# Performance work log

Measured on AMD Instinct MI355X. Metric: run time of the kernel, lower is better.

## Reference

```python
import jax, jax.numpy as jnp
import numpy as np

N = 50000      # nodes
E = 800000     # edges (before self-loops)
IN = 512       # in_dim
HID = 128      # hidden_dim
HEADS = 4
NEG_SLOPE = 0.2


def setup_inputs() -> dict:
    key = jax.random.key(0)
    ks = jax.random.split(key, 20)
    s = 0.05
    inp = {
        'x': jax.random.normal(ks[0], (N, IN), jnp.float32),
        'edge_index': jax.random.randint(ks[1], (2, E), 0, N, dtype=jnp.int32),
        # layer 0: GATConv(IN -> HID, heads=HEADS)
        'W0': jax.random.normal(ks[2], (HEADS * HID, IN), jnp.float32) * s,
        'a_src0': jax.random.normal(ks[3], (HEADS, HID), jnp.float32) * s,
        'a_dst0': jax.random.normal(ks[4], (HEADS, HID), jnp.float32) * s,
        'b0': jnp.zeros((HEADS * HID,), jnp.float32),
        # layer 1: GATConv(HEADS*HID -> HID, heads=HEADS)
        'W1': jax.random.normal(ks[5], (HEADS * HID, HEADS * HID), jnp.float32) * s,
        'a_src1': jax.random.normal(ks[6], (HEADS, HID), jnp.float32) * s,
        'a_dst1': jax.random.normal(ks[7], (HEADS, HID), jnp.float32) * s,
        'b1': jnp.zeros((HEADS * HID,), jnp.float32),
        # layer 2: GATConv(HEADS*HID -> HID, heads=1)
        'W2': jax.random.normal(ks[8], (HID, HEADS * HID), jnp.float32) * s,
        'a_src2': jax.random.normal(ks[9], (1, HID), jnp.float32) * s,
        'a_dst2': jax.random.normal(ks[10], (1, HID), jnp.float32) * s,
        'b2': jnp.zeros((HID,), jnp.float32),
        # output heads
        'Wv': jax.random.normal(ks[11], (HID, HID), jnp.float32) * s,
        'bv': jnp.zeros((HID,), jnp.float32),
        'Wt': jax.random.normal(ks[12], (HID, HID), jnp.float32) * s,
        'bt': jnp.zeros((HID,), jnp.float32),
    }
    return inp


def _gat_conv(x, src, dst, W, a_src, a_dst, bias, heads, n_nodes):
    """PyG-style GATConv (eval mode, att_dropout=0, self-loops pre-added)."""
    ch = a_src.shape[-1]
    h = (x @ W.T).reshape(n_nodes, heads, ch)            # [N,H,C]
    alpha_s = jnp.einsum('nhc,hc->nh', h, a_src)          # [N,H]
    alpha_d = jnp.einsum('nhc,hc->nh', h, a_dst)          # [N,H]
    e = alpha_s[src] + alpha_d[dst]                       # [E,H]
    e = jnp.where(e > 0, e, NEG_SLOPE * e)                # leaky_relu(0.2)
    # segment softmax over destination nodes
    m = jax.ops.segment_max(e, dst, num_segments=n_nodes)  # [N,H]
    e = jnp.exp(e - m[dst])
    z = jax.ops.segment_sum(e, dst, num_segments=n_nodes)  # [N,H]
    alpha = e / (z[dst] + 1e-16)                          # [E,H]
    msg = h[src] * alpha[:, :, None]                      # [E,H,C]
    out = jax.ops.segment_sum(msg, dst, num_segments=n_nodes)  # [N,H,C]
    return out.reshape(n_nodes, heads * ch) + bias


def reference(x, edge_index, W0, a_src0, a_dst0, b0, W1, a_src1, a_dst1, b1,
              W2, a_src2, a_dst2, b2, Wv, bv, Wt, bt):
    n = x.shape[0]
    loops = jnp.arange(n, dtype=edge_index.dtype)
    src = jnp.concatenate([edge_index[0], loops])
    dst = jnp.concatenate([edge_index[1], loops])

    h = _gat_conv(x, src, dst, W0, a_src0, a_dst0, b0, HEADS, n)
    h = jax.nn.relu(h)                                    # dropout is no-op in eval
    h = _gat_conv(h, src, dst, W1, a_src1, a_dst1, b1, HEADS, n)
    h = jax.nn.relu(h)
    h = _gat_conv(h, src, dst, W2, a_src2, a_dst2, b2, 1, n)  # [N,HID]

    x_vision = jax.nn.relu(h @ Wv.T + bv)
    x_text = jax.nn.relu(h @ Wt.T + bt)
    return (h, x_vision, x_text)
```

## Files before the change

### kernel.cpp

```cpp
#include <hip/hip_runtime.h>
#include <hip/hip_bf16.h>
#include <math.h>

typedef __bf16 bf16;
typedef __bf16 bf16x2 __attribute__((ext_vector_type(2)));
typedef __bf16 bf16x4 __attribute__((ext_vector_type(4)));
typedef __bf16 bf16x8 __attribute__((ext_vector_type(8)));
typedef float f32x4 __attribute__((ext_vector_type(4)));

#define NNODES 50000
#define NEDGES 800000

static __device__ __forceinline__ void gld_lds16(const void* g, void* l) {
    __builtin_amdgcn_global_load_lds((__attribute__((address_space(1))) void*)g,
                                     (__attribute__((address_space(3))) void*)l,
                                     16, 0, 0);
}

__global__ void detect_kernel(const unsigned int* __restrict__ xw, int* __restrict__ flag)
{
    const int l = threadIdx.x;
    int c = 0;
    for (int i = l; i < 4096; i += 64) {
        const unsigned int b1 = (xw[i] >> 8) & 0x7Fu;
        c += (b1 >= 0x34u && b1 <= 0x43u) ? 1 : 0;
    }
#pragma unroll
    for (int off = 32; off; off >>= 1) c += __shfl_xor(c, off);
    if (l == 0) *flag = (c < 2048) ? 1 : 0;
}

__global__ __launch_bounds__(256) void zero_out_kernel(void* out, long n, const int* __restrict__ flag)
{
    const int fp32 = *flag;
    const long i = (long)blockIdx.x * 256 + threadIdx.x;
    if (i < n) {
        if (fp32) ((float*)out)[i] = 0.f;
        else ((bf16*)out)[i] = (bf16)0.f;
    }
}

__global__ __launch_bounds__(256) void convert4_kernel(
    const void* __restrict__ in, bf16* __restrict__ out, int n4, const int* __restrict__ flag)
{
    const int fp32 = *flag;
    const int i = blockIdx.x * 256 + threadIdx.x;
    if (i >= n4) return;
    bf16x4 o;
    if (fp32) {
        const float4 v = ((const float4*)in)[i];
        o[0] = (bf16)v.x; o[1] = (bf16)v.y; o[2] = (bf16)v.z; o[3] = (bf16)v.w;
    } else {
        o = ((const bf16x4*)in)[i];
    }
    ((bf16x4*)out)[i] = o;
}

struct CvtBatch { const void* in[16]; bf16* out[16]; int n4[16]; };

__global__ __launch_bounds__(256) void convert_batch_kernel(CvtBatch b, const int* __restrict__ flag)
{
    const int fp32 = *flag;
    const int it = blockIdx.y;
    const int n4 = b.n4[it];
    const void* in = b.in[it];
    bf16* out = b.out[it];
    for (int i = blockIdx.x * 256 + threadIdx.x; i < n4; i += gridDim.x * 256) {
        bf16x4 o;
        if (fp32) {
            const float4 v = ((const float4*)in)[i];
            o[0] = (bf16)v.x; o[1] = (bf16)v.y; o[2] = (bf16)v.z; o[3] = (bf16)v.w;
        } else {
            o = ((const bf16x4*)in)[i];
        }
        ((bf16x4*)out)[i] = o;
    }
}

__global__ __launch_bounds__(256) void gemm_bt(
    const bf16* __restrict__ A, const bf16* __restrict__ B,
    bf16* __restrict__ C, int M, int N, int K,
    const bf16* __restrict__ av, const bf16* __restrict__ dv,
    float* __restrict__ aS, float* __restrict__ aD, int H)
{
    __shared__ __align__(16) bf16 As[128 * 32];
    __shared__ __align__(16) bf16 Bs[128 * 32];
    __shared__ float sPS[128];
    __shared__ float sPD[128];
    const int tid  = threadIdx.x;
    const int lane = tid & 63;
    const int w    = tid >> 6;
    const int wm   = (w >> 1) * 64, wn = (w & 1) * 64;
    const int mBase = blockIdx.y * 128, nBase = blockIdx.x * 128;
    const int hb = nBase >> 7;

    f32x4 acc[4][4];
#pragma unroll
    for (int i = 0; i < 4; i++)
#pragma unroll
        for (int j = 0; j < 4; j++)
#pragma unroll
            for (int r = 0; r < 4; r++) acc[i][j][r] = 0.f;

    const int rA   = tid >> 2;
    const int kseg = (tid & 3) * 8;
    int ra0 = mBase + rA;       if (ra0 > M - 1) ra0 = M - 1;
    int ra1 = mBase + rA + 64;  if (ra1 > M - 1) ra1 = M - 1;
    const bf16* gA0 = A + (long)ra0 * K + kseg;
    const bf16* gA1 = A + (long)ra1 * K + kseg;
    const bf16* gB0 = B + (long)(nBase + rA) * K + kseg;
    const bf16* gB1 = B + (long)(nBase + rA + 64) * K + kseg;
    bf16* lA0 = &As[tid * 8];
    bf16* lA1 = &As[(tid + 256) * 8];
    bf16* lB0 = &Bs[tid * 8];
    bf16* lB1 = &Bs[(tid + 256) * 8];

    const int quad = lane >> 4, l16 = lane & 15;

    if (tid < 128) { sPS[tid] = 0.f; sPD[tid] = 0.f; }

    for (int k0 = 0; k0 < K; k0 += 32) {
        gld_lds16(gA0 + k0, lA0);
        gld_lds16(gA1 + k0, lA1);
        gld_lds16(gB0 + k0, lB0);
        gld_lds16(gB1 + k0, lB1);
        __syncthreads();
        bf16x8 af[4], bfr[4];
#pragma unroll
        for (int i = 0; i < 4; i++) {
            af[i]  = *(const bf16x8*)&As[(wm + i * 16 + l16) * 32 + quad * 8];
            bfr[i] = *(const bf16x8*)&Bs[(wn + i * 16 + l16) * 32 + quad * 8];
        }
#pragma unroll
        for (int i = 0; i < 4; i++)
#pragma unroll
            for (int j = 0; j < 4; j++)
                acc[i][j] = __builtin_amdgcn_mfma_f32_16x16x32_bf16(af[i], bfr[j], acc[i][j], 0, 0, 0);
        __syncthreads();
    }

    float aval[4], dval[4];
#pragma unroll
    for (int j = 0; j < 4; j++) {
        const int cg = nBase + wn + j * 16 + l16;
        aval[j] = (float)av[cg];
        dval[j] = (float)dv[cg];
    }
#pragma unroll
    for (int i = 0; i < 4; i++) {
#pragma unroll
        for (int r = 0; r < 4; r++) {
            float ps = 0.f, pd = 0.f;
#pragma unroll
            for (int j = 0; j < 4; j++) {
                ps += acc[i][j][r] * aval[j];
                pd += acc[i][j][r] * dval[j];
            }
#pragma unroll
            for (int off = 8; off; off >>= 1) {
                ps += __shfl_xor(ps, off);
                pd += __shfl_xor(pd, off);
            }
            if (l16 == 0) {
                const int rl = wm + i * 16 + quad * 4 + r;
                atomicAdd(&sPS[rl], ps);
                atomicAdd(&sPD[rl], pd);
            }
        }
    }

#pragma unroll
    for (int i = 0; i < 4; i++) {
        const int row0 = mBase + wm + i * 16 + quad * 4;
#pragma unroll
        for (int j = 0; j < 4; j++) {
            const int colg = nBase + wn + j * 16 + l16;
#pragma unroll
            for (int r = 0; r < 4; r++) {
                const int row = row0 + r;
                if (row < M) C[(long)row * N + colg] = (bf16)acc[i][j][r];
            }
        }
    }

    __syncthreads();
    if (tid < 128) {
        const int row = mBase + tid;
        if (row < M) {
            aS[(long)row * H + hb] = sPS[tid];
            aD[(long)row * H + hb] = sPD[tid];
        }
    }
}

__global__ void hist_kernel(const int* __restrict__ dst, int* __restrict__ cnt, int E)
{
    const int e = blockIdx.x * blockDim.x + threadIdx.x;
    if (e < E) atomicAdd(&cnt[dst[e]], 1);
}

__global__ __launch_bounds__(256) void scan1_kernel(
    const int* __restrict__ cnt, int* __restrict__ rowptr, int* __restrict__ blksum, int n)
{
    __shared__ int buf[256];
    const int b = blockIdx.x, t = threadIdx.x, i = b * 256 + t;
    const int v = (i < n) ? cnt[i] : 0;
    buf[t] = v;
    __syncthreads();
    for (int off = 1; off < 256; off <<= 1) {
        const int add = (t >= off) ? buf[t - off] : 0;
        __syncthreads();
        buf[t] += add;
        __syncthreads();
    }
    if (i < n) rowptr[i + 1] = buf[t];
    if (t == 255) blksum[b] = buf[255];
    if (b == 0 && t == 0) rowptr[0] = 0;
}

__global__ __launch_bounds__(256) void scan2_kernel(int* __restrict__ blksum, int nb)
{
    __shared__ int buf[256];
    const int t = threadIdx.x;
    const int v = (t < nb) ? blksum[t] : 0;
    buf[t] = v;
    __syncthreads();
    for (int off = 1; off < 256; off <<= 1) {
        const int add = (t >= off) ? buf[t - off] : 0;
        __syncthreads();
        buf[t] += add;
        __syncthreads();
    }
    if (t < nb) blksum[t] = buf[t] - v;
}

__global__ __launch_bounds__(256) void scan3_kernel(
    int* __restrict__ rowptr, const int* __restrict__ blksum, int n)
{
    const int b = blockIdx.x, i = b * 256 + threadIdx.x;
    if (i < n) rowptr[i + 1] += blksum[b];
}

__global__ void fill_kernel(const int* __restrict__ src, const int* __restrict__ dst,
                            const int* __restrict__ rowptr, int* __restrict__ off,
                            int* __restrict__ col, int E)
{
    const int e = blockIdx.x * blockDim.x + threadIdx.x;
    if (e < E) {
        const int d = dst[e];
        const int p = rowptr[d] + atomicAdd(&off[d], 1);
        col[p] = src[e];
    }
}

__global__ __launch_bounds__(256) void agg4s_kernel(
    const bf16* __restrict__ h, const float* __restrict__ asrc,
    const float* __restrict__ adst, const int* __restrict__ rowptr,
    const int* __restrict__ col, const bf16* __restrict__ bias,
    bf16* __restrict__ out, int NB)
{
    __shared__ int2 ew_s[4][64];
    const int w = threadIdx.x >> 6, lane = threadIdx.x & 63;
    const int g = lane >> 4, li = lane & 15;
    const int xcd = blockIdx.x & 7;
    const int s = xcd >> 1;
    const int nbi = ((blockIdx.x >> 3) << 1) | (xcd & 1);
    const int n = nbi * 4 + w;
    const float ad = adst[(long)n * 4 + s];
    const int start = rowptr[n];
    const int deg   = rowptr[n + 1] - start;
    const int total = deg + 1;

    float z = 0.f;
    float acc[8];
#pragma unroll
    for (int c = 0; c < 8; c++) acc[c] = 0.f;
    const char* hbp = (const char*)h;
    const int sOff = s * 256 + li * 16;
    const int2* ews = ew_s[w];

    for (int base = 0; base < total; base += 64) {
        const int i = base + lane;
        const bool valid = i < total;
        const int sv = (i < deg) ? col[start + i] : n;
        float e = asrc[(long)sv * 4 + s] + ad;
        e = (e > 0.f) ? e : 0.2f * e;
        e = fminf(fmaxf(e, -60.f), 60.f);
        const float wv = valid ? __expf(e) : 0.f;
        ew_s[w][lane] = make_int2(sv << 10, __float_as_int(wv));
        __builtin_amdgcn_wave_barrier();
        const int cnt = min(64, total - base);
#pragma unroll 2
        for (int j = 0; j < cnt; j += 4) {
            const int2 v = ews[j + g];
            const float ww = __int_as_float(v.y);
            z += ww;
            const bf16x8 hv = *(const bf16x8*)(hbp + (v.x + sOff));
#pragma unroll
            for (int c = 0; c < 8; c++) acc[c] += ww * (float)hv[c];
        }
        __builtin_amdgcn_wave_barrier();
    }

#pragma unroll
    for (int c = 0; c < 8; c++) {
        acc[c] += __shfl_xor(acc[c], 16);
        acc[c] += __shfl_xor(acc[c], 32);
    }
    z += __shfl_xor(z, 16);
    z += __shfl_xor(z, 32);

    if (g == 0) {
        const float rz = 1.f / (z + 1e-16f);
        const bf16x8 b8 = *(const bf16x8*)(bias + s * 128 + li * 8);
        bf16x8 ov;
#pragma unroll
        for (int c = 0; c < 8; c++)
            ov[c] = (bf16)fmaxf(acc[c] * rz + (float)b8[c], 0.f);
        *(bf16x8*)(out + (long)n * 512 + s * 128 + li * 8) = ov;
    }
}

__global__ __launch_bounds__(256) void agg1g_kernel(
    const bf16* __restrict__ h, const float* __restrict__ asrc,
    const float* __restrict__ adst, const int* __restrict__ rowptr,
    const int* __restrict__ col, const bf16* __restrict__ bias,
    void* __restrict__ outv, const int* __restrict__ dflag)
{
    __shared__ int2 ew_s[4][64];
    const int w = threadIdx.x >> 6, lane = threadIdx.x & 63;
    const int g = lane >> 4, li = lane & 15;
    const int n = blockIdx.x * 4 + w;
    if (n >= NNODES) return;
    const int fp32out = *dflag;
    const float ad = adst[n];
    const int start = rowptr[n];
    const int deg   = rowptr[n + 1] - start;
    const int total = deg + 1;

    float z = 0.f;
    float acc[8];
#pragma unroll
    for (int c = 0; c < 8; c++) acc[c] = 0.f;
    const char* hbp = (const char*)h;
    const int sOff = li * 16;
    const int2* ews = ew_s[w];

    for (int base = 0; base < total; base += 64) {
        const int i = base + lane;
        const bool valid = i < total;
        const int sv = (i < deg) ? col[start + i] : n;
        float e = asrc[sv] + ad;
        e = (e > 0.f) ? e : 0.2f * e;
        e = fminf(fmaxf(e, -60.f), 60.f);
        const float wv = valid ? __expf(e) : 0.f;
        ew_s[w][lane] = make_int2(sv << 8, __float_as_int(wv));
        __builtin_amdgcn_wave_barrier();
        const int cnt = min(64, total - base);
#pragma unroll 2
        for (int j = 0; j < cnt; j += 4) {
            const int2 v = ews[j + g];
            const float ww = __int_as_float(v.y);
            z += ww;
            const bf16x8 hv = *(const bf16x8*)(hbp + (v.x + sOff));
#pragma unroll
            for (int c = 0; c < 8; c++) acc[c] += ww * (float)hv[c];
        }
        __builtin_amdgcn_wave_barrier();
    }

#pragma unroll
    for (int c = 0; c < 8; c++) {
        acc[c] += __shfl_xor(acc[c], 16);
        acc[c] += __shfl_xor(acc[c], 32);
    }
    z += __shfl_xor(z, 16);
    z += __shfl_xor(z, 32);

    if (g == 0) {
        const float rz = 1.f / (z + 1e-16f);
        float o[8];
#pragma unroll
        for (int c = 0; c < 8; c++)
            o[c] = acc[c] * rz + (float)bias[li * 8 + c];
        if (fp32out) {
            float* op = (float*)outv + (long)n * 128 + li * 8;
            f32x4 o0, o1;
#pragma unroll
            for (int c = 0; c < 4; c++) { o0[c] = o[c]; o1[c] = o[c + 4]; }
            *(f32x4*)op = o0;
            *(f32x4*)(op + 4) = o1;
        } else {
            bf16x8 ov;
#pragma unroll
            for (int c = 0; c < 8; c++) ov[c] = (bf16)o[c];
            *(bf16x8*)((bf16*)outv + (long)n * 128 + li * 8) = ov;
        }
    }
}

__global__ __launch_bounds__(256) void heads_kernel(
    const void* __restrict__ hbase, void* __restrict__ outv,
    const bf16* __restrict__ Wv, const bf16* __restrict__ bv,
    const bf16* __restrict__ Wt, const bf16* __restrict__ bt,
    const int* __restrict__ dflag, int N)
{
    const int fp32 = *dflag;
    __shared__ float hbuf[32][128];
    const int n0 = blockIdx.x * 32, t = threadIdx.x;
    for (int i = t; i < 32 * 128; i += 256) {
        const int node = n0 + (i >> 7), c = i & 127;
        float v = 0.f;
        if (node < N)
            v = fp32 ? ((const float*)hbase)[(long)node * 128 + c]
                     : (float)((const bf16*)hbase)[(long)node * 128 + c];
        hbuf[i >> 7][c] = v;
    }
    __syncthreads();
    const int m = t & 127;
    const bool vis = t < 128;
    const bf16* W = vis ? Wv : Wt;
    const float b = (float)(vis ? bv[m] : bt[m]);
    float acc[32];
#pragma unroll
    for (int i = 0; i < 32; i++) acc[i] = 0.f;
    for (int k0 = 0; k0 < 128; k0 += 8) {
        const bf16x8 wv8 = *(const bf16x8*)&W[m * 128 + k0];
#pragma unroll
        for (int kk = 0; kk < 8; kk++) {
            const float wk = (float)wv8[kk];
#pragma unroll
            for (int i = 0; i < 32; i++) acc[i] += hbuf[i][k0 + kk] * wk;
        }
    }
    const long sec = vis ? (long)N * 128 : (long)2 * N * 128;
#pragma unroll
    for (int i = 0; i < 32; i++) {
        const int node = n0 + i;
        if (node < N) {
            float o = fmaxf(acc[i] + b, 0.f);
            const long idx = sec + (long)node * 128 + m;
            if (fp32) ((float*)outv)[idx] = o;
            else ((bf16*)outv)[idx] = (bf16)o;
        }
    }
}

extern "C" void kernel_launch(void* const* d_in, const int* in_sizes, int n_in,
                              void* d_out, int out_size, void* d_ws, size_t ws_size,
                              hipStream_t stream)
{
    const int N = NNODES, E = NEDGES;
    const int* srcp = (const int*)d_in[1];
    const int* dstp = srcp + E;

    char* p0 = (char*)d_ws;
    char* p = p0;
    auto bump = [&](size_t b) { char* r = p; p += (b + 255) & ~(size_t)255; return r; };
    int*   dflag  = (int*)bump(256);
    bf16*  xc     = (bf16*)bump((size_t)N * 512 * 2);
    bf16*  W0c    = (bf16*)bump(262144 * 2);
    bf16*  as0c   = (bf16*)bump(512 * 2);
    bf16*  ad0c   = (bf16*)bump(512 * 2);
    bf16*  b0c    = (bf16*)bump(512 * 2);
    bf16*  W1c    = (bf16*)bump(262144 * 2);
    bf16*  as1c   = (bf16*)bump(512 * 2);
    bf16*  ad1c   = (bf16*)bump(512 * 2);
    bf16*  b1c    = (bf16*)bump(512 * 2);
    bf16*  W2c    = (bf16*)bump(65536 * 2);
    bf16*  as2c   = (bf16*)bump(128 * 2);
    bf16*  ad2c   = (bf16*)bump(128 * 2);
    bf16*  b2c    = (bf16*)bump(128 * 2);
    bf16*  Wvc    = (bf16*)bump(16384 * 2);
    bf16*  bvc    = (bf16*)bump(128 * 2);
    bf16*  Wtc    = (bf16*)bump(16384 * 2);
    bf16*  btc    = (bf16*)bump(128 * 2);
    int*   cnt    = (int*)bump((size_t)N * 4);
    int*   offs   = (int*)bump((size_t)N * 4);
    int*   rowptr = (int*)bump((size_t)(N + 1) * 4);
    int*   blksum = (int*)bump(256 * 4);
    int*   colarr = (int*)bump((size_t)E * 4);
    float* alphaS = (float*)bump((size_t)N * 4 * 4);
    float* alphaD = (float*)bump((size_t)N * 4 * 4);
    bf16*  bufA   = (bf16*)bump((size_t)N * 512 * 2);
    bf16*  bufB   = (bf16*)bump((size_t)N * 512 * 2);
    const size_t need = (size_t)(p - p0);

    detect_kernel<<<1, 64, 0, stream>>>((const unsigned int*)d_in[0], dflag);

    if (need > ws_size) {
        zero_out_kernel<<<((long)out_size + 255) / 256, 256, 0, stream>>>(d_out, out_size, dflag);
        return;
    }

    convert4_kernel<<<(N * 512 / 4 + 255) / 256, 256, 0, stream>>>(d_in[0], xc, N * 512 / 4, dflag);
    CvtBatch cb;
    const void* ins[16] = {d_in[2], d_in[3], d_in[4], d_in[5], d_in[6], d_in[7], d_in[8], d_in[9],
                           d_in[10], d_in[11], d_in[12], d_in[13], d_in[14], d_in[15], d_in[16], d_in[17]};
    bf16* outs[16] = {W0c, as0c, ad0c, b0c, W1c, as1c, ad1c, b1c,
                      W2c, as2c, ad2c, b2c, Wvc, bvc, Wtc, btc};
    const int ns4[16] = {65536, 128, 128, 128, 65536, 128, 128, 128,
                         16384, 32, 32, 32, 4096, 32, 4096, 32};
    for (int i = 0; i < 16; i++) { cb.in[i] = ins[i]; cb.out[i] = outs[i]; cb.n4[i] = ns4[i]; }
    convert_batch_kernel<<<dim3(64, 16), 256, 0, stream>>>(cb, dflag);

    const int nb = (N + 255) / 256;
    hipMemsetAsync(cnt, 0, (size_t)N * 4, stream);
    hipMemsetAsync(offs, 0, (size_t)N * 4, stream);
    hist_kernel<<<(E + 255) / 256, 256, 0, stream>>>(dstp, cnt, E);
    scan1_kernel<<<nb, 256, 0, stream>>>(cnt, rowptr, blksum, N);
    scan2_kernel<<<1, 256, 0, stream>>>(blksum, nb);
    scan3_kernel<<<nb, 256, 0, stream>>>(rowptr, blksum, N);
    fill_kernel<<<(E + 255) / 256, 256, 0, stream>>>(srcp, dstp, rowptr, offs, colarr, E);

    const int NB = N / 4;

    dim3 g0(4, (N + 127) / 128);
    gemm_bt<<<g0, 256, 0, stream>>>(xc, W0c, bufA, N, 512, 512,
                                    as0c, ad0c, alphaS, alphaD, 4);
    agg4s_kernel<<<NB * 4, 256, 0, stream>>>(bufA, alphaS, alphaD, rowptr, colarr, b0c, bufB, NB);

    gemm_bt<<<g0, 256, 0, stream>>>(bufB, W1c, bufA, N, 512, 512,
                                    as1c, ad1c, alphaS, alphaD, 4);
    agg4s_kernel<<<NB * 4, 256, 0, stream>>>(bufA, alphaS, alphaD, rowptr, colarr, b1c, bufB, NB);

    dim3 g2(1, (N + 127) / 128);
    gemm_bt<<<g2, 256, 0, stream>>>(bufB, W2c, bufA, N, 128, 512,
                                    as2c, ad2c, alphaS, alphaD, 1);
    agg1g_kernel<<<(N + 3) / 4, 256, 0, stream>>>(bufA, alphaS, alphaD, rowptr, colarr, b2c, d_out, dflag);

    heads_kernel<<<(N + 31) / 32, 256, 0, stream>>>(d_out, d_out, Wvc, bvc, Wtc, btc, dflag, N);
}
```

Measured before the change: 797.5 us.

## Store GEMM output in 32-column slab layout and split aggregation into 32-channel slices

The GEMM epilogue now writes its output in a slab-major layout: 32-column slabs, each laid out contiguously over all nodes. The aggregation kernels then give each block one 32-channel slice (16 slices for 4 heads, 4 for 1 head), mapped to XCDs by block index. Each slice's gathered working set (64 bytes per node) is much smaller and can stay resident in the per-XCD L2, which is meant to cut repeated random gathers from HBM. The cost is that the edge-weight computation is redundantly repeated across slices, there are more launches of blocks, and the extra shuffle reductions add work.

```diff
diff --git a/kernel.cpp b/kernel.cpp
--- a/kernel.cpp
+++ b/kernel.cpp
@@ -170,15 +170,16 @@
     }
 
 #pragma unroll
-    for (int i = 0; i < 4; i++) {
-        const int row0 = mBase + wm + i * 16 + quad * 4;
-#pragma unroll
-        for (int j = 0; j < 4; j++) {
-            const int colg = nBase + wn + j * 16 + l16;
+    for (int j = 0; j < 4; j++) {
+        const int colg = nBase + wn + j * 16 + l16;
+        const long sbase = (long)(colg >> 5) * M * 32 + (colg & 31);
+#pragma unroll
+        for (int i = 0; i < 4; i++) {
+            const int row0 = mBase + wm + i * 16 + quad * 4;
 #pragma unroll
             for (int r = 0; r < 4; r++) {
                 const int row = row0 + r;
-                if (row < M) C[(long)row * N + colg] = (bf16)acc[i][j][r];
+                if (row < M) C[sbase + (long)row * 32] = (bf16)acc[i][j][r];
             }
         }
     }
@@ -261,12 +262,15 @@
 {
     __shared__ int2 ew_s[4][64];
     const int w = threadIdx.x >> 6, lane = threadIdx.x & 63;
-    const int g = lane >> 4, li = lane & 15;
+    const int g = lane >> 2, li = lane & 3;
     const int xcd = blockIdx.x & 7;
-    const int s = xcd >> 1;
-    const int nbi = ((blockIdx.x >> 3) << 1) | (xcd & 1);
-    const int n = nbi * 4 + w;
-    const float ad = adst[(long)n * 4 + s];
+    const int r0 = blockIdx.x >> 3;
+    const int half = (r0 >= NB) ? 1 : 0;
+    const int i0 = r0 - half * NB;
+    const int s = half * 8 + xcd;
+    const int head = s >> 2;
+    const int n = i0 * 4 + w;
+    const float ad = adst[(long)n * 4 + head];
     const int start = rowptr[n];
     const int deg   = rowptr[n + 1] - start;
     const int total = deg + 1;
@@ -276,22 +280,21 @@
 #pragma unroll
     for (int c = 0; c < 8; c++) acc[c] = 0.f;
     const char* hbp = (const char*)h;
-    const int sOff = s * 256 + li * 16;
+    const int sOff = s * (NNODES * 64) + li * 16;
     const int2* ews = ew_s[w];
 
     for (int base = 0; base < total; base += 64) {
         const int i = base + lane;
         const bool valid = i < total;
         const int sv = (i < deg) ? col[start + i] : n;
-        float e = asrc[(long)sv * 4 + s] + ad;
+        float e = asrc[(long)sv * 4 + head] + ad;
         e = (e > 0.f) ? e : 0.2f * e;
         e = fminf(fmaxf(e, -60.f), 60.f);
         const float wv = valid ? __expf(e) : 0.f;
-        ew_s[w][lane] = make_int2(sv << 10, __float_as_int(wv));
+        ew_s[w][lane] = make_int2(sv << 6, __float_as_int(wv));
         __builtin_amdgcn_wave_barrier();
         const int cnt = min(64, total - base);
-#pragma unroll 2
-        for (int j = 0; j < cnt; j += 4) {
+        for (int j = 0; j < cnt; j += 16) {
             const int2 v = ews[j + g];
             const float ww = __int_as_float(v.y);
             z += ww;
@@ -304,20 +307,24 @@
 
 #pragma unroll
     for (int c = 0; c < 8; c++) {
+        acc[c] += __shfl_xor(acc[c], 4);
+        acc[c] += __shfl_xor(acc[c], 8);
         acc[c] += __shfl_xor(acc[c], 16);
         acc[c] += __shfl_xor(acc[c], 32);
     }
+    z += __shfl_xor(z, 4);
+    z += __shfl_xor(z, 8);
     z += __shfl_xor(z, 16);
     z += __shfl_xor(z, 32);
 
-    if (g == 0) {
+    if (lane < 4) {
         const float rz = 1.f / (z + 1e-16f);
-        const bf16x8 b8 = *(const bf16x8*)(bias + s * 128 + li * 8);
+        const bf16x8 b8 = *(const bf16x8*)(bias + s * 32 + li * 8);
         bf16x8 ov;
 #pragma unroll
         for (int c = 0; c < 8; c++)
             ov[c] = (bf16)fmaxf(acc[c] * rz + (float)b8[c], 0.f);
-        *(bf16x8*)(out + (long)n * 512 + s * 128 + li * 8) = ov;
+        *(bf16x8*)(out + (long)n * 512 + s * 32 + li * 8) = ov;
     }
 }
 
@@ -329,9 +336,11 @@
 {
     __shared__ int2 ew_s[4][64];
     const int w = threadIdx.x >> 6, lane = threadIdx.x & 63;
-    const int g = lane >> 4, li = lane & 15;
-    const int n = blockIdx.x * 4 + w;
-    if (n >= NNODES) return;
+    const int g = lane >> 2, li = lane & 3;
+    const int xcd = blockIdx.x & 7;
+    const int s = xcd >> 1;
+    const int nbi = ((blockIdx.x >> 3) << 1) | (xcd & 1);
+    const int n = nbi * 4 + w;
     const int fp32out = *dflag;
     const float ad = adst[n];
     const int start = rowptr[n];
@@ -343,7 +352,7 @@
 #pragma unroll
     for (int c = 0; c < 8; c++) acc[c] = 0.f;
     const char* hbp = (const char*)h;
-    const int sOff = li * 16;
+    const int sOff = s * (NNODES * 64) + li * 16;
     const int2* ews = ew_s[w];
 
     for (int base = 0; base < total; base += 64) {
@@ -354,11 +363,10 @@
         e = (e > 0.f) ? e : 0.2f * e;
         e = fminf(fmaxf(e, -60.f), 60.f);
         const float wv = valid ? __expf(e) : 0.f;
-        ew_s[w][lane] = make_int2(sv << 8, __float_as_int(wv));
+        ew_s[w][lane] = make_int2(sv << 6, __float_as_int(wv));
         __builtin_amdgcn_wave_barrier();
         const int cnt = min(64, total - base);
-#pragma unroll 2
-        for (int j = 0; j < cnt; j += 4) {
+        for (int j = 0; j < cnt; j += 16) {
             const int2 v = ews[j + g];
             const float ww = __int_as_float(v.y);
             z += ww;
@@ -371,20 +379,24 @@
 
 #pragma unroll
     for (int c = 0; c < 8; c++) {
+        acc[c] += __shfl_xor(acc[c], 4);
+        acc[c] += __shfl_xor(acc[c], 8);
         acc[c] += __shfl_xor(acc[c], 16);
         acc[c] += __shfl_xor(acc[c], 32);
     }
+    z += __shfl_xor(z, 4);
+    z += __shfl_xor(z, 8);
     z += __shfl_xor(z, 16);
     z += __shfl_xor(z, 32);
 
-    if (g == 0) {
+    if (lane < 4) {
         const float rz = 1.f / (z + 1e-16f);
         float o[8];
 #pragma unroll
         for (int c = 0; c < 8; c++)
-            o[c] = acc[c] * rz + (float)bias[li * 8 + c];
+            o[c] = acc[c] * rz + (float)bias[s * 32 + li * 8 + c];
         if (fp32out) {
-            float* op = (float*)outv + (long)n * 128 + li * 8;
+            float* op = (float*)outv + (long)n * 128 + s * 32 + li * 8;
             f32x4 o0, o1;
 #pragma unroll
             for (int c = 0; c < 4; c++) { o0[c] = o[c]; o1[c] = o[c + 4]; }
@@ -394,7 +406,7 @@
             bf16x8 ov;
 #pragma unroll
             for (int c = 0; c < 8; c++) ov[c] = (bf16)o[c];
-            *(bf16x8*)((bf16*)outv + (long)n * 128 + li * 8) = ov;
+            *(bf16x8*)((bf16*)outv + (long)n * 128 + s * 32 + li * 8) = ov;
         }
     }
 }
@@ -518,16 +530,16 @@
     dim3 g0(4, (N + 127) / 128);
     gemm_bt<<<g0, 256, 0, stream>>>(xc, W0c, bufA, N, 512, 512,
                                     as0c, ad0c, alphaS, alphaD, 4);
-    agg4s_kernel<<<NB * 4, 256, 0, stream>>>(bufA, alphaS, alphaD, rowptr, colarr, b0c, bufB, NB);
+    agg4s_kernel<<<NB * 16, 256, 0, stream>>>(bufA, alphaS, alphaD, rowptr, colarr, b0c, bufB, NB);
 
     gemm_bt<<<g0, 256, 0, stream>>>(bufB, W1c, bufA, N, 512, 512,
                                     as1c, ad1c, alphaS, alphaD, 4);
-    agg4s_kernel<<<NB * 4, 256, 0, stream>>>(bufA, alphaS, alphaD, rowptr, colarr, b1c, bufB, NB);
+    agg4s_kernel<<<NB * 16, 256, 0, stream>>>(bufA, alphaS, alphaD, rowptr, colarr, b1c, bufB, NB);
 
     dim3 g2(1, (N + 127) / 128);
     gemm_bt<<<g2, 256, 0, stream>>>(bufB, W2c, bufA, N, 128, 512,
                                     as2c, ad2c, alphaS, alphaD, 1);
-    agg1g_kernel<<<(N + 3) / 4, 256, 0, stream>>>(bufA, alphaS, alphaD, rowptr, colarr, b2c, d_out, dflag);
+    agg1g_kernel<<<(NB / 2) * 8, 256, 0, stream>>>(bufA, alphaS, alphaD, rowptr, colarr, b2c, d_out, dflag);
 
     heads_kernel<<<(N + 31) / 32, 256, 0, stream>>>(d_out, d_out, Wvc, bvc, Wtc, btc, dflag, N);
 }
```

After: 1.265 ms. 58.6% more time.
